# Kernel optimization log

Hardware: AMD Instinct MI355X
Metric: run time of the kernel (lower is better)

## Reference

```python
import jax, jax.numpy as jnp
import numpy as np

D = 4                      # corr_disp / max_displacement
K = 2 * D + 1              # window side -> K*K = 81 displacement channels
C = 256                    # in_channels


def shifted_patches(x, d):
    """x: [B,C,H,W] -> [B,C,K*K,H,W]; patch k=(dy*K+dx) is x shifted by
    (dy-d, dx-d) with zero padding (matches Correlation/NaiveAssemble2 indexing)."""
    B, Ch, H, W = x.shape
    xp = jnp.pad(x, ((0, 0), (0, 0), (d, d), (d, d)))
    k = 2 * d + 1
    sl = [xp[:, :, dy:dy + H, dx:dx + W] for dy in range(k) for dx in range(k)]
    return jnp.stack(sl, axis=2)


def conv2d(x, w, b, pad):
    y = jax.lax.conv_general_dilated(
        x, w, window_strides=(1, 1), padding=[(pad, pad), (pad, pad)],
        dimension_numbers=('NCHW', 'OIHW', 'NCHW'))
    return y + b[None, :, None, None]


def setup_inputs() -> dict:
    key = jax.random.key(0)
    ks = jax.random.split(key, 12)
    B, H, W = 2, 64, 64
    std = 0.01
    return {
        'feat':     jax.random.normal(ks[0], (B, C, H, W), jnp.float32),
        'feat_ref': jax.random.normal(ks[1], (B, C, H, W), jnp.float32),
        # ConcatUpdate conv stack: 2C->256 (1x1), 256->16 (3x3), 16->3 (3x3), 3->2 (3x3)
        'w1': jax.random.normal(ks[2], (256, 2 * C, 1, 1), jnp.float32) * std,
        'b1': jnp.zeros((256,), jnp.float32),
        'w2': jax.random.normal(ks[3], (16, 256, 3, 3), jnp.float32) * std,
        'b2': jnp.zeros((16,), jnp.float32),
        'w3': jax.random.normal(ks[4], (3, 16, 3, 3), jnp.float32) * std,
        'b3': jnp.zeros((3,), jnp.float32),
        'w4': jax.random.normal(ks[5], (2, 3, 3, 3), jnp.float32) * std,
        'b4': jnp.array([1.0, 0.0], jnp.float32),  # init_weights: bias[0]=1, bias[1]=0
    }


def reference(feat, feat_ref, w1, b1, w2, b2, w3, b3, w4, b4):
    # Correlation (cost volume over (2D+1)^2 displacements, kernel_size=1)
    patches = shifted_patches(feat_ref, D)                    # [B,C,K2,H,W]
    aff = jnp.einsum('bchw,bckhw->bkhw', feat, patches)       # [B,K2,H,W]
    # sum-normalize over displacement channels (use_softmax_norm=False)
    aff = aff / (jnp.sum(aff, axis=1, keepdims=True) + 1e-7)
    # NaiveAssemble2: windowed weighted gather of feat_ref
    aligned = jnp.einsum('bkhw,bckhw->bchw', aff, patches)    # [B,C,H,W]
    # ConcatUpdate
    cat = jnp.concatenate([feat, aligned], axis=1)            # [B,2C,H,W]
    h = conv2d(cat, w1, b1, 0)
    h = conv2d(h, w2, b2, 1)
    h = conv2d(h, w3, b3, 1)
    logits = conv2d(h, w4, b4, 1)                             # [B,2,H,W]
    score = jax.nn.softmax(logits, axis=1)
    return score[:, 0:1] * feat + score[:, 1:2] * aligned
```

## Files before the change

### kernel.cpp

```cpp
#include <hip/hip_runtime.h>
#include <hip/hip_bf16.h>
#include <math.h>

#define BATCH 2
#define CCH   256
#define HH    64
#define WW    64
#define PIX   (HH*WW)
#define K2    81
#define BP_N  (BATCH*PIX)

__global__ void k_transpose(const float* __restrict__ in, float* __restrict__ out) {
    __shared__ float tile[32][33];
    int b  = blockIdx.z;
    int p0 = blockIdx.x * 32;
    int c0 = blockIdx.y * 32;
    int tx = threadIdx.x;
    int ty = threadIdx.y;
    const float* ib = in  + (size_t)b * CCH * PIX;
    float*       ob = out + (size_t)b * CCH * PIX;
    #pragma unroll
    for (int i = 0; i < 4; i++) {
        int c = c0 + ty + i * 8;
        int p = p0 + tx;
        tile[ty + i * 8][tx] = ib[(size_t)c * PIX + p];
    }
    __syncthreads();
    #pragma unroll
    for (int i = 0; i < 4; i++) {
        int p = p0 + ty + i * 8;
        int c = c0 + tx;
        ob[(size_t)p * CCH + c] = tile[tx][ty + i * 8];
    }
}

__global__ void k_corr_assemble(const float* __restrict__ featT,
                                const float* __restrict__ refT,
                                float* __restrict__ alignedT) {
    int blk = blockIdx.x;
    int bp  = ((blk & 7) << 10) | (blk >> 3);
    int b  = bp >> 12;
    int p  = bp & 4095;
    int h  = p >> 6, w = p & 63;
    int tid = threadIdx.x;

    __shared__ float s_aff[K2];
    __shared__ int   s_pix[K2];
    __shared__ __align__(16) float s_affc[88];
    __shared__ __align__(16) int   s_poff[88];
    __shared__ int   s_kc[88];
    __shared__ int   s_kc_hi[24];
    __shared__ int   s_cnt0, s_cnt1;
    __shared__ float s_den;

    if (tid < K2) {
        s_aff[tid] = 0.f;
        int dy = tid / 9, dx = tid - dy * 9;
        int y = h + dy - 4, x = w + dx - 4;
        s_pix[tid] = ((unsigned)y < 64u && (unsigned)x < 64u) ? ((y << 6) | x) : -1;
    }
    __syncthreads();

    if (tid < 128) {
        bool valid = (tid < K2) && (s_pix[tid] >= 0);
        unsigned long long m = __ballot(valid);
        int lane   = tid & 63;
        int prefix = __popcll(m & ((1ULL << lane) - 1ULL));
        if (tid < 64) {
            if (valid) s_kc[prefix] = tid;
            if (tid == 0) s_cnt0 = (int)__popcll(m);
        } else {
            if (valid) s_kc_hi[prefix] = tid;
            if (tid == 64) s_cnt1 = (int)__popcll(m);
        }
    }
    __syncthreads();
    int n0 = s_cnt0, n1 = s_cnt1;
    int nv = n0 + n1;
    if (tid < n1) s_kc[n0 + tid] = s_kc_hi[tid];
    __syncthreads();
    if (tid < nv) s_poff[tid] = s_pix[s_kc[tid]] << 10;
    __syncthreads();

    const float* rb = refT + ((size_t)b << 20);

    int hw = tid >> 5;
    int j  = tid & 31;
    const float* fb = featT + ((size_t)bp << 8) + j;
    float f[8];
    #pragma unroll
    for (int t = 0; t < 8; t++) f[t] = fb[32 * t];

    for (int ii = hw; ii < nv; ii += 8) {
        int k    = s_kc[ii];
        int poff = s_poff[ii];
        const char* rp = (const char*)rb + poff + 4 * j;
        float partial = 0.f;
        #pragma unroll
        for (int t = 0; t < 8; t++)
            partial = fmaf(f[t], *(const float*)(rp + 128 * t), partial);
        partial = __fadd_rn(partial, __shfl_xor(partial, 8));
        partial = __fadd_rn(partial, __shfl_xor(partial, 16));
        partial = __fadd_rn(partial, __shfl_xor(partial, 4));
        partial = __fadd_rn(partial, __shfl_xor(partial, 2));
        partial = __fadd_rn(partial, __shfl_xor(partial, 1));
        if (j == 0) s_aff[k] = partial;
    }
    __syncthreads();

    if (tid == 0) {
        float s = 0.f;
        for (int k = 0; k < K2; k++) s = __fadd_rn(s, s_aff[k]);
        s_den = __fadd_rn(s, 1e-7f);
    }
    __syncthreads();
    if (tid < nv) s_affc[tid] = __fdiv_rn(s_aff[s_kc[tid]], s_den);
    __syncthreads();

    const char* rbc = (const char*)rb + ((size_t)tid << 2);
    float acc = 0.f;
    int i = 0;
    for (; i + 4 <= nv; i += 4) {
        float4 af = *(const float4*)&s_affc[i];
        int4   po = *(const int4*)&s_poff[i];
        float v0 = *(const float*)(rbc + po.x);
        float v1 = *(const float*)(rbc + po.y);
        float v2 = *(const float*)(rbc + po.z);
        float v3 = *(const float*)(rbc + po.w);
        acc = fmaf(af.x, v0, acc);
        acc = fmaf(af.y, v1, acc);
        acc = fmaf(af.z, v2, acc);
        acc = fmaf(af.w, v3, acc);
    }
    for (; i < nv; i++)
        acc = fmaf(s_affc[i], *(const float*)(rbc + s_poff[i]), acc);
    alignedT[((size_t)bp << 8) + tid] = acc;
}

__global__ void k_w1t(const float* __restrict__ w1, float* __restrict__ w1t) {
    __shared__ float tile[32][33];
    int c0 = blockIdx.x * 32;
    int o0 = blockIdx.y * 32;
    int tx = threadIdx.x;
    int ty = threadIdx.y;
    #pragma unroll
    for (int i = 0; i < 4; i++)
        tile[ty + i * 8][tx] = w1[(size_t)(o0 + ty + i * 8) * 512 + c0 + tx];
    __syncthreads();
    #pragma unroll
    for (int i = 0; i < 4; i++)
        w1t[(size_t)(c0 + ty + i * 8) * 256 + o0 + tx] = tile[tx][ty + i * 8];
}

__global__ void k_conv1(const float* __restrict__ featT,
                        const float* __restrict__ alignedT,
                        const float* __restrict__ w1t,
                        const float* __restrict__ b1,
                        float* __restrict__ h1) {
    __shared__ float s_a[32][68];
    __shared__ float s_b[32][68];
    int m0  = blockIdx.x * 64;
    int n0  = blockIdx.y * 64;
    int tid = threadIdx.x;
    int tx  = tid & 15;
    int ty  = tid >> 4;

    float acc[4][4] = {{0.f}};

    for (int kc = 0; kc < 16; kc++) {
        int c0 = kc * 32;
        const float* asrc;
        int coff;
        if (c0 < 256) { asrc = featT;    coff = c0; }
        else          { asrc = alignedT; coff = c0 - 256; }

        #pragma unroll
        for (int i = tid; i < 512; i += 256) {
            int cq = i & 7, px = i >> 3;
            float4 v = *(const float4*)(asrc + ((size_t)(m0 + px) << 8) + coff + (cq << 2));
            s_a[cq * 4 + 0][px] = v.x;
            s_a[cq * 4 + 1][px] = v.y;
            s_a[cq * 4 + 2][px] = v.z;
            s_a[cq * 4 + 3][px] = v.w;
        }
        #pragma unroll
        for (int i = tid; i < 512; i += 256) {
            int oq = i & 15, cc = i >> 4;
            float4 v = *(const float4*)(w1t + (size_t)(c0 + cc) * 256 + n0 + (oq << 2));
            *(float4*)&s_b[cc][oq << 2] = v;
        }
        __syncthreads();

        #pragma unroll 8
        for (int k = 0; k < 32; k++) {
            float4 av = *(const float4*)&s_a[k][ty << 2];
            float4 bv = *(const float4*)&s_b[k][tx << 2];
            acc[0][0] = fmaf(av.x, bv.x, acc[0][0]);
            acc[0][1] = fmaf(av.x, bv.y, acc[0][1]);
            acc[0][2] = fmaf(av.x, bv.z, acc[0][2]);
            acc[0][3] = fmaf(av.x, bv.w, acc[0][3]);
            acc[1][0] = fmaf(av.y, bv.x, acc[1][0]);
            acc[1][1] = fmaf(av.y, bv.y, acc[1][1]);
            acc[1][2] = fmaf(av.y, bv.z, acc[1][2]);
            acc[1][3] = fmaf(av.y, bv.w, acc[1][3]);
            acc[2][0] = fmaf(av.z, bv.x, acc[2][0]);
            acc[2][1] = fmaf(av.z, bv.y, acc[2][1]);
            acc[2][2] = fmaf(av.z, bv.z, acc[2][2]);
            acc[2][3] = fmaf(av.z, bv.w, acc[2][3]);
            acc[3][0] = fmaf(av.w, bv.x, acc[3][0]);
            acc[3][1] = fmaf(av.w, bv.y, acc[3][1]);
            acc[3][2] = fmaf(av.w, bv.z, acc[3][2]);
            acc[3][3] = fmaf(av.w, bv.w, acc[3][3]);
        }
        __syncthreads();
    }

    float4 bias = *(const float4*)(b1 + n0 + tx * 4);
    #pragma unroll
    for (int i = 0; i < 4; i++) {
        int px = m0 + ty * 4 + i;
        float4 v;
        v.x = acc[i][0] + bias.x;
        v.y = acc[i][1] + bias.y;
        v.z = acc[i][2] + bias.z;
        v.w = acc[i][3] + bias.w;
        *(float4*)(h1 + ((size_t)px << 8) + n0 + tx * 4) = v;
    }
}

__global__ void k_w2t(const float* __restrict__ w2, float* __restrict__ w2t) {
    int i = blockIdx.x * 256 + threadIdx.x;
    if (i >= 16 * 256 * 9) return;
    int o  = i / 2304;
    int r  = i % 2304;
    int c  = r / 9;
    int kk = r % 9;
    int cg = c >> 2, ci = c & 3;
    w2t[(((kk * 64 + cg) * 16 + o) << 2) + ci] = w2[i];
}

__global__ void k_conv2(const float* __restrict__ h1,
                        const float* __restrict__ w2t,
                        const float* __restrict__ b2,
                        float* __restrict__ h2) {
    __shared__ float s_in[3][18][68];
    int blk = blockIdx.x;
    int b   = blk >> 8;
    int r   = blk & 255;
    int y   = r >> 2;
    int w0  = (r & 3) * 16;
    int tid = threadIdx.x;
    int o   = tid & 15;
    int ps  = (tid >> 4) & 7;

    const float* hb = h1 + ((size_t)b << 20);

    float4 a0 = {0.f, 0.f, 0.f, 0.f};
    float4 a1 = {0.f, 0.f, 0.f, 0.f};

    for (int chunk = 0; chunk < 4; chunk++) {
        int c0 = chunk << 6;
        for (int i = tid; i < 3 * 18 * 16; i += 256) {
            int c4 = i & 15;
            int pi = (i >> 4) % 18;
            int ri = (i >> 4) / 18;
            int yy = y + ri - 1;
            int xx = w0 + pi - 1;
            float4 v = {0.f, 0.f, 0.f, 0.f};
            if ((unsigned)yy < 64u && (unsigned)xx < 64u)
                v = *(const float4*)(hb + ((size_t)((yy << 6) | xx) << 8) + c0 + (c4 << 2));
            *(float4*)&s_in[ri][pi][c4 << 2] = v;
        }
        __syncthreads();

        #pragma unroll
        for (int kk = 0; kk < 9; kk++) {
            int ky = kk / 3, kx = kk - ky * 3;
            const float* wp = w2t + (((size_t)(kk * 64 + (c0 >> 2)) * 16 + o) << 2);
            #pragma unroll 8
            for (int c4 = 0; c4 < 16; c4++) {
                float4 wv = *(const float4*)(wp + (c4 << 6));
                float4 i0 = *(const float4*)&s_in[ky][ps + kx][c4 << 2];
                float4 i1 = *(const float4*)&s_in[ky][ps + 8 + kx][c4 << 2];
                a0.x = fmaf(wv.x, i0.x, a0.x);
                a0.y = fmaf(wv.y, i0.y, a0.y);
                a0.z = fmaf(wv.z, i0.z, a0.z);
                a0.w = fmaf(wv.w, i0.w, a0.w);
                a1.x = fmaf(wv.x, i1.x, a1.x);
                a1.y = fmaf(wv.y, i1.y, a1.y);
                a1.z = fmaf(wv.z, i1.z, a1.z);
                a1.w = fmaf(wv.w, i1.w, a1.w);
            }
        }
        __syncthreads();
    }

    size_t bp0 = ((size_t)b << 12) + (y << 6) + w0;
    h2[(bp0 + ps) * 16 + o]     = ((a0.x + a0.y) + (a0.z + a0.w)) + b2[o];
    h2[(bp0 + ps + 8) * 16 + o] = ((a1.x + a1.y) + (a1.z + a1.w)) + b2[o];
}

__global__ void k_conv3(const float* __restrict__ h2,
                        const float* __restrict__ w3,
                        const float* __restrict__ b3,
                        float* __restrict__ h3) {
    int bp = blockIdx.x * 256 + threadIdx.x;
    if (bp >= BP_N) return;
    int b = bp >> 12;
    int p = bp & 4095;
    int h = p >> 6, w = p & 63;
    const float* hb = h2 + ((size_t)b << 16);

    float a0 = 0.f, a1 = 0.f, a2 = 0.f;
    #pragma unroll
    for (int kk = 0; kk < 9; kk++) {
        int ky = kk / 3, kx = kk - ky * 3;
        int y = h + ky - 1, x = w + kx - 1;
        if ((unsigned)y >= 64u || (unsigned)x >= 64u) continue;
        const float* ip = hb + (size_t)((y << 6) | x) * 16;
        #pragma unroll
        for (int c = 0; c < 16; c++) {
            float v = ip[c];
            int wi = c * 9 + kk;
            a0 = fmaf(w3[wi],       v, a0);
            a1 = fmaf(w3[144 + wi], v, a1);
            a2 = fmaf(w3[288 + wi], v, a2);
        }
    }
    h3[(size_t)bp * 3 + 0] = a0 + b3[0];
    h3[(size_t)bp * 3 + 1] = a1 + b3[1];
    h3[(size_t)bp * 3 + 2] = a2 + b3[2];
}

__global__ void k_score(const float* __restrict__ h3,
                        const float* __restrict__ w4,
                        const float* __restrict__ b4,
                        float2* __restrict__ score) {
    int bp = blockIdx.x * 256 + threadIdx.x;
    if (bp >= BP_N) return;
    int b = bp >> 12;
    int p = bp & 4095;
    int h = p >> 6, w = p & 63;
    const float* hb = h3 + (size_t)b * PIX * 3;

    float l0 = 0.f, l1 = 0.f;
    #pragma unroll
    for (int kk = 0; kk < 9; kk++) {
        int ky = kk / 3, kx = kk - ky * 3;
        int y = h + ky - 1, x = w + kx - 1;
        if ((unsigned)y >= 64u || (unsigned)x >= 64u) continue;
        const float* ip = hb + (size_t)((y << 6) | x) * 3;
        #pragma unroll
        for (int c = 0; c < 3; c++) {
            float v = ip[c];
            int wi = c * 9 + kk;
            l0 = fmaf(w4[wi],      v, l0);
            l1 = fmaf(w4[27 + wi], v, l1);
        }
    }
    l0 += b4[0];
    l1 += b4[1];

    float m  = fmaxf(l0, l1);
    float e0 = expf(l0 - m);
    float e1 = expf(l1 - m);
    float s  = e0 + e1;
    score[bp] = make_float2(e0 / s, e1 / s);
}

__global__ void k_blend(const float* __restrict__ feat,
                        const float* __restrict__ alignedT,
                        const float2* __restrict__ score,
                        float* __restrict__ out) {
    __shared__ float tile[32][33];
    int b  = blockIdx.z;
    int p0 = blockIdx.x * 32;
    int c0 = blockIdx.y * 32;
    int tx = threadIdx.x;
    int ty = threadIdx.y;

    const float* at = alignedT + ((size_t)b << 20);
    #pragma unroll
    for (int i = 0; i < 4; i++) {
        int p = p0 + ty + i * 8;
        tile[ty + i * 8][tx] = at[((size_t)p << 8) + c0 + tx];
    }
    __syncthreads();

    int p = p0 + tx;
    float2 s = score[(b << 12) + p];
    #pragma unroll
    for (int i = 0; i < 4; i++) {
        int c = c0 + ty + i * 8;
        size_t idx = (((size_t)(b * 256 + c)) << 12) + p;
        out[idx] = __fadd_rn(__fmul_rn(s.x, feat[idx]),
                             __fmul_rn(s.y, tile[tx][ty + i * 8]));
    }
}

extern "C" void kernel_launch(void* const* d_in, const int* in_sizes, int n_in,
                              void* d_out, int out_size, void* d_ws, size_t ws_size,
                              hipStream_t stream) {
    const float* feat     = (const float*)d_in[0];
    const float* feat_ref = (const float*)d_in[1];
    const float* w1 = (const float*)d_in[2];
    const float* b1 = (const float*)d_in[3];
    const float* w2 = (const float*)d_in[4];
    const float* b2 = (const float*)d_in[5];
    const float* w3 = (const float*)d_in[6];
    const float* b3 = (const float*)d_in[7];
    const float* w4 = (const float*)d_in[8];
    const float* b4 = (const float*)d_in[9];
    float* out = (float*)d_out;

    const size_t NCP = (size_t)BATCH * CCH * PIX;
    char* wsb = (char*)d_ws;
    float*  featT    = (float*)wsb;   wsb += NCP * 4;
    float*  refT     = (float*)wsb;   wsb += NCP * 4;
    float*  alignedT = (float*)wsb;   wsb += NCP * 4;
    float*  h1       = (float*)wsb;   wsb += NCP * 4;
    float*  h2       = (float*)wsb;   wsb += (size_t)BP_N * 16 * 4;
    float*  h3       = (float*)wsb;   wsb += (size_t)BP_N * 3 * 4;
    float2* sc       = (float2*)wsb;  wsb += (size_t)BP_N * 8;
    float*  w2t      = (float*)wsb;   wsb += (size_t)16 * 256 * 9 * 4;
    float*  w1t      = (float*)wsb;   wsb += (size_t)512 * 256 * 4;

    dim3 tb(32, 8, 1);
    dim3 tg(PIX / 32, CCH / 32, BATCH);
    k_transpose<<<tg, tb, 0, stream>>>(feat, featT);
    k_transpose<<<tg, tb, 0, stream>>>(feat_ref, refT);
    k_w2t<<<144, 256, 0, stream>>>(w2, w2t);
    k_w1t<<<dim3(16, 8, 1), tb, 0, stream>>>(w1, w1t);

    k_corr_assemble<<<BP_N, 256, 0, stream>>>(featT, refT, alignedT);
    k_conv1<<<dim3(BP_N / 64, 256 / 64, 1), 256, 0, stream>>>(featT, alignedT, w1t, b1, h1);
    k_conv2<<<BP_N / 16, 256, 0, stream>>>(h1, w2t, b2, h2);
    k_conv3<<<BP_N / 256, 256, 0, stream>>>(h2, w3, b3, h3);
    k_score<<<BP_N / 256, 256, 0, stream>>>(h3, w4, b4, sc);
    k_blend<<<tg, tb, 0, stream>>>(feat, alignedT, sc, out);
}
```

Before: 232.2 us.

## Process two adjacent pixels per correlation block and merge prep kernels

The correlation/assemble kernel now handles two horizontally adjacent pixels per block. It iterates over a 9x10 union window so each refT row load feeds both pixels' dot products and both weighted gathers. This halves the block count and reuses reference loads across neighbours, at the cost of more registers and more complex index bookkeeping. The two transposes are also merged into one launch, and the two weight-prep kernels into another, to cut launch overhead.

```diff
diff --git a/kernel.cpp b/kernel.cpp
--- a/kernel.cpp
+++ b/kernel.cpp
@@ -10,9 +10,15 @@
 #define K2    81
 #define BP_N  (BATCH*PIX)
 
-__global__ void k_transpose(const float* __restrict__ in, float* __restrict__ out) {
+__global__ void k_transpose2(const float* __restrict__ feat,
+                             const float* __restrict__ feat_ref,
+                             float* __restrict__ featT,
+                             float* __restrict__ refT) {
     __shared__ float tile[32][33];
-    int b  = blockIdx.z;
+    int z  = blockIdx.z;
+    int b  = z & 1;
+    const float* in  = (z >> 1) ? feat_ref : feat;
+    float*       out = (z >> 1) ? refT     : featT;
     int p0 = blockIdx.x * 32;
     int c0 = blockIdx.y * 32;
     int tx = threadIdx.x;
@@ -34,122 +40,214 @@
     }
 }
 
+__global__ void k_wprep(const float* __restrict__ w1, float* __restrict__ w1t,
+                        const float* __restrict__ w2, float* __restrict__ w2t) {
+    __shared__ float tile[32][33];
+    int blk = blockIdx.x;
+    int tid = threadIdx.x;
+    if (blk < 128) {
+        int c0 = (blk & 15) * 32;
+        int o0 = (blk >> 4) * 32;
+        int tx = tid & 31;
+        int ty = tid >> 5;
+        #pragma unroll
+        for (int i = 0; i < 4; i++)
+            tile[ty + i * 8][tx] = w1[(size_t)(o0 + ty + i * 8) * 512 + c0 + tx];
+        __syncthreads();
+        #pragma unroll
+        for (int i = 0; i < 4; i++)
+            w1t[(size_t)(c0 + ty + i * 8) * 256 + o0 + tx] = tile[tx][ty + i * 8];
+    } else {
+        int i = (blk - 128) * 256 + tid;
+        if (i < 16 * 256 * 9) {
+            int o  = i / 2304;
+            int r  = i % 2304;
+            int c  = r / 9;
+            int kk = r % 9;
+            int cg = c >> 2, ci = c & 3;
+            w2t[(((kk * 64 + cg) * 16 + o) << 2) + ci] = w2[i];
+        }
+    }
+}
+
 __global__ void k_corr_assemble(const float* __restrict__ featT,
                                 const float* __restrict__ refT,
                                 float* __restrict__ alignedT) {
     int blk = blockIdx.x;
-    int bp  = ((blk & 7) << 10) | (blk >> 3);
+    int pr  = ((blk & 7) << 9) | (blk >> 3);
+    int bp  = pr << 1;
     int b  = bp >> 12;
     int p  = bp & 4095;
     int h  = p >> 6, w = p & 63;
     int tid = threadIdx.x;
 
-    __shared__ float s_aff[K2];
-    __shared__ int   s_pix[K2];
-    __shared__ __align__(16) float s_affc[88];
-    __shared__ __align__(16) int   s_poff[88];
-    __shared__ int   s_kc[88];
-    __shared__ int   s_kc_hi[24];
+    __shared__ float s_aff0[K2];
+    __shared__ float s_aff1[K2];
+    __shared__ __align__(8) int2 s_u[96];
+    __shared__ int   s_hi_a[32];
+    __shared__ int   s_hi_b[32];
     __shared__ int   s_cnt0, s_cnt1;
-    __shared__ float s_den;
-
-    if (tid < K2) {
-        s_aff[tid] = 0.f;
-        int dy = tid / 9, dx = tid - dy * 9;
-        int y = h + dy - 4, x = w + dx - 4;
-        s_pix[tid] = ((unsigned)y < 64u && (unsigned)x < 64u) ? ((y << 6) | x) : -1;
-    }
-    __syncthreads();
+    __shared__ float s_den0, s_den1;
+    __shared__ __align__(16) float s_c0[96];
+    __shared__ __align__(16) float s_c1[96];
+    __shared__ __align__(16) int   s_po[96];
+
+    int hw = tid >> 5;
+    int j  = tid & 31;
+
+    const float* fb = featT + ((size_t)bp << 8) + j;
+    float f0[8], f1[8];
+    #pragma unroll
+    for (int t = 0; t < 8; t++) { f0[t] = fb[32 * t]; f1[t] = fb[256 + 32 * t]; }
+
+    if (tid < K2) { s_aff0[tid] = 0.f; s_aff1[tid] = 0.f; }
 
     if (tid < 128) {
-        bool valid = (tid < K2) && (s_pix[tid] >= 0);
+        int u  = tid;
+        int uy = u / 10, ux = u - uy * 10;
+        int y  = h + uy - 4, x = w + ux - 4;
+        bool valid = (u < 90) && ((unsigned)y < 64u) && ((unsigned)x < 64u);
+        int poff = ((y << 6) | x) << 10;
+        int meta = (ux << 8) | (uy * 9 + ux);
         unsigned long long m = __ballot(valid);
         int lane   = tid & 63;
         int prefix = __popcll(m & ((1ULL << lane) - 1ULL));
         if (tid < 64) {
-            if (valid) s_kc[prefix] = tid;
+            if (valid) s_u[prefix] = make_int2(poff, meta);
             if (tid == 0) s_cnt0 = (int)__popcll(m);
         } else {
-            if (valid) s_kc_hi[prefix] = tid;
+            if (valid) { s_hi_a[prefix] = poff; s_hi_b[prefix] = meta; }
             if (tid == 64) s_cnt1 = (int)__popcll(m);
         }
     }
     __syncthreads();
     int n0 = s_cnt0, n1 = s_cnt1;
-    int nv = n0 + n1;
-    if (tid < n1) s_kc[n0 + tid] = s_kc_hi[tid];
-    __syncthreads();
-    if (tid < nv) s_poff[tid] = s_pix[s_kc[tid]] << 10;
-    __syncthreads();
-
-    const float* rb = refT + ((size_t)b << 20);
-
-    int hw = tid >> 5;
-    int j  = tid & 31;
-    const float* fb = featT + ((size_t)bp << 8) + j;
-    float f[8];
-    #pragma unroll
-    for (int t = 0; t < 8; t++) f[t] = fb[32 * t];
-
-    for (int ii = hw; ii < nv; ii += 8) {
-        int k    = s_kc[ii];
-        int poff = s_poff[ii];
-        const char* rp = (const char*)rb + poff + 4 * j;
-        float partial = 0.f;
-        #pragma unroll
-        for (int t = 0; t < 8; t++)
-            partial = fmaf(f[t], *(const float*)(rp + 128 * t), partial);
-        partial = __fadd_rn(partial, __shfl_xor(partial, 8));
-        partial = __fadd_rn(partial, __shfl_xor(partial, 16));
-        partial = __fadd_rn(partial, __shfl_xor(partial, 4));
-        partial = __fadd_rn(partial, __shfl_xor(partial, 2));
-        partial = __fadd_rn(partial, __shfl_xor(partial, 1));
-        if (j == 0) s_aff[k] = partial;
-    }
-    __syncthreads();
-
-    if (tid == 0) {
+    int nu = n0 + n1;
+    if (tid < n1) s_u[n0 + tid] = make_int2(s_hi_a[tid], s_hi_b[tid]);
+    __syncthreads();
+
+    const float* rb  = refT + ((size_t)b << 20);
+    const char*  rbj = (const char*)rb + 4 * j;
+
+    for (int ii = 2 * hw; ii < nu; ii += 16) {
+        int2 U0 = s_u[ii];
+        bool has1 = (ii + 1) < nu;
+        int2 U1 = has1 ? s_u[ii + 1] : U0;
+        const char* rp0 = rbj + U0.x;
+        const char* rp1 = rbj + U1.x;
+        float r0[8], r1[8];
+        #pragma unroll
+        for (int t = 0; t < 8; t++) {
+            r0[t] = *(const float*)(rp0 + 128 * t);
+            r1[t] = *(const float*)(rp1 + 128 * t);
+        }
+        float pa0 = 0.f, pb0 = 0.f, pa1 = 0.f, pb1 = 0.f;
+        #pragma unroll
+        for (int t = 0; t < 8; t++) {
+            pa0 = fmaf(f0[t], r0[t], pa0);
+            pb0 = fmaf(f1[t], r0[t], pb0);
+            pa1 = fmaf(f0[t], r1[t], pa1);
+            pb1 = fmaf(f1[t], r1[t], pb1);
+        }
+        pa0 = __fadd_rn(pa0, __shfl_xor(pa0, 8));
+        pb0 = __fadd_rn(pb0, __shfl_xor(pb0, 8));
+        pa1 = __fadd_rn(pa1, __shfl_xor(pa1, 8));
+        pb1 = __fadd_rn(pb1, __shfl_xor(pb1, 8));
+        pa0 = __fadd_rn(pa0, __shfl_xor(pa0, 16));
+        pb0 = __fadd_rn(pb0, __shfl_xor(pb0, 16));
+        pa1 = __fadd_rn(pa1, __shfl_xor(pa1, 16));
+        pb1 = __fadd_rn(pb1, __shfl_xor(pb1, 16));
+        pa0 = __fadd_rn(pa0, __shfl_xor(pa0, 4));
+        pb0 = __fadd_rn(pb0, __shfl_xor(pb0, 4));
+        pa1 = __fadd_rn(pa1, __shfl_xor(pa1, 4));
+        pb1 = __fadd_rn(pb1, __shfl_xor(pb1, 4));
+        pa0 = __fadd_rn(pa0, __shfl_xor(pa0, 2));
+        pb0 = __fadd_rn(pb0, __shfl_xor(pb0, 2));
+        pa1 = __fadd_rn(pa1, __shfl_xor(pa1, 2));
+        pb1 = __fadd_rn(pb1, __shfl_xor(pb1, 2));
+        pa0 = __fadd_rn(pa0, __shfl_xor(pa0, 1));
+        pb0 = __fadd_rn(pb0, __shfl_xor(pb0, 1));
+        pa1 = __fadd_rn(pa1, __shfl_xor(pa1, 1));
+        pb1 = __fadd_rn(pb1, __shfl_xor(pb1, 1));
+        if (j == 0) {
+            int k0 = U0.y & 255, ux0 = U0.y >> 8;
+            if (ux0 < 9) s_aff0[k0] = pa0;
+            if (ux0 > 0) s_aff1[k0 - 1] = pb0;
+            if (has1) {
+                int k1 = U1.y & 255, ux1 = U1.y >> 8;
+                if (ux1 < 9) s_aff0[k1] = pa1;
+                if (ux1 > 0) s_aff1[k1 - 1] = pb1;
+            }
+        }
+    }
+    __syncthreads();
+
+    if (tid < 2) {
+        const float* sa = tid ? s_aff1 : s_aff0;
         float s = 0.f;
-        for (int k = 0; k < K2; k++) s = __fadd_rn(s, s_aff[k]);
-        s_den = __fadd_rn(s, 1e-7f);
-    }
-    __syncthreads();
-    if (tid < nv) s_affc[tid] = __fdiv_rn(s_aff[s_kc[tid]], s_den);
+        for (int k = 0; k < K2; k++) s = __fadd_rn(s, sa[k]);
+        float d = __fadd_rn(s, 1e-7f);
+        if (tid) s_den1 = d; else s_den0 = d;
+    }
+    __syncthreads();
+
+    if (tid < nu) {
+        int2 uu = s_u[tid];
+        int k0 = uu.y & 255, ux = uu.y >> 8;
+        s_po[tid] = uu.x;
+        s_c0[tid] = (ux < 9) ? __fdiv_rn(s_aff0[k0], s_den0) : 0.f;
+        s_c1[tid] = (ux > 0) ? __fdiv_rn(s_aff1[k0 - 1], s_den1) : 0.f;
+    }
     __syncthreads();
 
     const char* rbc = (const char*)rb + ((size_t)tid << 2);
-    float acc = 0.f;
+    float a0 = 0.f, a1 = 0.f;
     int i = 0;
-    for (; i + 4 <= nv; i += 4) {
-        float4 af = *(const float4*)&s_affc[i];
-        int4   po = *(const int4*)&s_poff[i];
+    for (; i + 8 <= nu; i += 8) {
+        float4 cA0 = *(const float4*)&s_c0[i];
+        float4 cA1 = *(const float4*)&s_c0[i + 4];
+        float4 cB0 = *(const float4*)&s_c1[i];
+        float4 cB1 = *(const float4*)&s_c1[i + 4];
+        int4   poA = *(const int4*)&s_po[i];
+        int4   poB = *(const int4*)&s_po[i + 4];
+        float v0 = *(const float*)(rbc + poA.x);
+        float v1 = *(const float*)(rbc + poA.y);
+        float v2 = *(const float*)(rbc + poA.z);
+        float v3 = *(const float*)(rbc + poA.w);
+        float v4 = *(const float*)(rbc + poB.x);
+        float v5 = *(const float*)(rbc + poB.y);
+        float v6 = *(const float*)(rbc + poB.z);
+        float v7 = *(const float*)(rbc + poB.w);
+        a0 = fmaf(cA0.x, v0, a0);  a1 = fmaf(cB0.x, v0, a1);
+        a0 = fmaf(cA0.y, v1, a0);  a1 = fmaf(cB0.y, v1, a1);
+        a0 = fmaf(cA0.z, v2, a0);  a1 = fmaf(cB0.z, v2, a1);
+        a0 = fmaf(cA0.w, v3, a0);  a1 = fmaf(cB0.w, v3, a1);
+        a0 = fmaf(cA1.x, v4, a0);  a1 = fmaf(cB1.x, v4, a1);
+        a0 = fmaf(cA1.y, v5, a0);  a1 = fmaf(cB1.y, v5, a1);
+        a0 = fmaf(cA1.z, v6, a0);  a1 = fmaf(cB1.z, v6, a1);
+        a0 = fmaf(cA1.w, v7, a0);  a1 = fmaf(cB1.w, v7, a1);
+    }
+    if (i + 4 <= nu) {
+        float4 cA = *(const float4*)&s_c0[i];
+        float4 cB = *(const float4*)&s_c1[i];
+        int4   po = *(const int4*)&s_po[i];
         float v0 = *(const float*)(rbc + po.x);
         float v1 = *(const float*)(rbc + po.y);
         float v2 = *(const float*)(rbc + po.z);
         float v3 = *(const float*)(rbc + po.w);
-        acc = fmaf(af.x, v0, acc);
-        acc = fmaf(af.y, v1, acc);
-        acc = fmaf(af.z, v2, acc);
-        acc = fmaf(af.w, v3, acc);
-    }
-    for (; i < nv; i++)
-        acc = fmaf(s_affc[i], *(const float*)(rbc + s_poff[i]), acc);
-    alignedT[((size_t)bp << 8) + tid] = acc;
-}
-
-__global__ void k_w1t(const float* __restrict__ w1, float* __restrict__ w1t) {
-    __shared__ float tile[32][33];
-    int c0 = blockIdx.x * 32;
-    int o0 = blockIdx.y * 32;
-    int tx = threadIdx.x;
-    int ty = threadIdx.y;
-    #pragma unroll
-    for (int i = 0; i < 4; i++)
-        tile[ty + i * 8][tx] = w1[(size_t)(o0 + ty + i * 8) * 512 + c0 + tx];
-    __syncthreads();
-    #pragma unroll
-    for (int i = 0; i < 4; i++)
-        w1t[(size_t)(c0 + ty + i * 8) * 256 + o0 + tx] = tile[tx][ty + i * 8];
+        a0 = fmaf(cA.x, v0, a0);  a1 = fmaf(cB.x, v0, a1);
+        a0 = fmaf(cA.y, v1, a0);  a1 = fmaf(cB.y, v1, a1);
+        a0 = fmaf(cA.z, v2, a0);  a1 = fmaf(cB.z, v2, a1);
+        a0 = fmaf(cA.w, v3, a0);  a1 = fmaf(cB.w, v3, a1);
+        i += 4;
+    }
+    for (; i < nu; i++) {
+        float v = *(const float*)(rbc + s_po[i]);
+        a0 = fmaf(s_c0[i], v, a0);
+        a1 = fmaf(s_c1[i], v, a1);
+    }
+    alignedT[((size_t)bp << 8) + tid]       = a0;
+    alignedT[((size_t)(bp + 1) << 8) + tid] = a1;
 }
 
 __global__ void k_conv1(const float* __restrict__ featT,
@@ -228,17 +326,6 @@
     }
 }
 
-__global__ void k_w2t(const float* __restrict__ w2, float* __restrict__ w2t) {
-    int i = blockIdx.x * 256 + threadIdx.x;
-    if (i >= 16 * 256 * 9) return;
-    int o  = i / 2304;
-    int r  = i % 2304;
-    int c  = r / 9;
-    int kk = r % 9;
-    int cg = c >> 2, ci = c & 3;
-    w2t[(((kk * 64 + cg) * 16 + o) << 2) + ci] = w2[i];
-}
-
 __global__ void k_conv2(const float* __restrict__ h1,
                         const float* __restrict__ w2t,
                         const float* __restrict__ b2,
@@ -426,16 +513,13 @@
     float*  w1t      = (float*)wsb;   wsb += (size_t)512 * 256 * 4;
 
     dim3 tb(32, 8, 1);
-    dim3 tg(PIX / 32, CCH / 32, BATCH);
-    k_transpose<<<tg, tb, 0, stream>>>(feat, featT);
-    k_transpose<<<tg, tb, 0, stream>>>(feat_ref, refT);
-    k_w2t<<<144, 256, 0, stream>>>(w2, w2t);
-    k_w1t<<<dim3(16, 8, 1), tb, 0, stream>>>(w1, w1t);
-
-    k_corr_assemble<<<BP_N, 256, 0, stream>>>(featT, refT, alignedT);
+    k_transpose2<<<dim3(PIX / 32, CCH / 32, 4), tb, 0, stream>>>(feat, feat_ref, featT, refT);
+    k_wprep<<<272, 256, 0, stream>>>(w1, w1t, w2, w2t);
+
+    k_corr_assemble<<<BP_N / 2, 256, 0, stream>>>(featT, refT, alignedT);
     k_conv1<<<dim3(BP_N / 64, 256 / 64, 1), 256, 0, stream>>>(featT, alignedT, w1t, b1, h1);
     k_conv2<<<BP_N / 16, 256, 0, stream>>>(h1, w2t, b2, h2);
     k_conv3<<<BP_N / 256, 256, 0, stream>>>(h2, w3, b3, h3);
     k_score<<<BP_N / 256, 256, 0, stream>>>(h3, w4, b4, sc);
-    k_blend<<<tg, tb, 0, stream>>>(feat, alignedT, sc, out);
-}
+    k_blend<<<dim3(PIX / 32, CCH / 32, BATCH), tb, 0, stream>>>(feat, alignedT, sc, out);
+}
```

Measured after the change: 221.8 us. 4.5% less time.
